# Kernel optimization log

Hardware: AMD Instinct MI355X
Metric: run time of the kernel (lower is better)

## Reference

```python
import jax, jax.numpy as jnp
import numpy as np

EPS = 1e-12

def _l2norm(x, axis=-1):
    n = jnp.sqrt(jnp.sum(x * x, axis=axis, keepdims=True))
    return x / jnp.maximum(n, EPS)

def setup_inputs() -> dict:
    key = jax.random.key(0)
    kq, kk, kv = jax.random.split(key, 3)
    N, K, D = 512, 262144, 256
    query = jax.random.normal(kq, (N, D), dtype=jnp.float32)
    # buffers are initialized as row-normalized gaussians in __init__
    queue_k = _l2norm(jax.random.normal(kk, (K, D), dtype=jnp.float32), axis=1)
    queue_v = _l2norm(jax.random.normal(kv, (K, D), dtype=jnp.float32), axis=1)
    return {"query": query, "queue_k": queue_k, "queue_v": queue_v}

TOP_N = 32

def reference(query, queue_k, queue_v):
    q = _l2norm(query.astype(jnp.float32), axis=1)          # [N, D]
    similarity = jnp.einsum('nd,kd->nk', q, queue_k)        # [N, K]
    _, topk_indices = jax.lax.top_k(similarity, TOP_N)      # [N, top_n]
    get_k = queue_k[topk_indices]                           # [N, top_n, D]
    get_v = queue_v[topk_indices]                           # [N, top_n, D]
    return (get_k, get_v)
```

## Files before the change

kernel.cpp:

```cpp
#include <hip/hip_runtime.h>
#include <hip/hip_bf16.h>

#define NQ     512
#define KTOT   262144
#define DD     256
#define TK     32
#define LSTR   264
#define NCHUNK 512
#define CHUNK  (KTOT / NCHUNK)
#define NTILE  (CHUNK / TK)
#define EMIT_T 0.189f
#define CAP    896
#define QCAP   8
#define NSLOT  (CAP / 64)
#define SEL    64
#define TOPN   32

typedef __bf16 bf16x8 __attribute__((ext_vector_type(8)));
typedef __bf16 bf16x4 __attribute__((ext_vector_type(4)));
typedef float  f32x4  __attribute__((ext_vector_type(4)));

__global__ void prep_kernel(const float* __restrict__ query,
                            __bf16* __restrict__ qn, int* __restrict__ cnt) {
    int q = blockIdx.x, l = threadIdx.x;
    f32x4 v = *(const f32x4*)&query[q * DD + l * 4];
    float ss = v.x*v.x + v.y*v.y + v.z*v.z + v.w*v.w;
    #pragma unroll
    for (int off = 32; off; off >>= 1) ss += __shfl_xor(ss, off);
    float s = rsqrtf(fmaxf(ss, 1e-24f));
    bf16x4 o = { (__bf16)(v.x * s), (__bf16)(v.y * s),
                 (__bf16)(v.z * s), (__bf16)(v.w * s) };
    *(bf16x4*)&qn[q * DD + l * 4] = o;
    if (l == 0) cnt[q] = 0;
}

__global__ __launch_bounds__(1024, 4)
void phase1_kernel(const __bf16* __restrict__ qn, const float* __restrict__ qk,
                   int* __restrict__ cnt, float* __restrict__ csc,
                   int* __restrict__ cix) {
    __shared__ __bf16 lds_k[2][TK * LSTR];
    __shared__ int    lcnt[NQ];
    __shared__ float  lsc[NQ][QCAP];
    __shared__ int    lkey[NQ][QCAP];
    const int tid  = threadIdx.x;
    const int lane = tid & 63, w = tid >> 6;
    const int am   = lane & 15, aq4 = lane >> 4;
    const size_t kbase = (size_t)blockIdx.x * CHUNK;
    const float* kp = &qk[kbase * DD];

    if (tid < NQ) lcnt[tid] = 0;

    bf16x8 areg[2][8];
    #pragma unroll
    for (int a = 0; a < 2; ++a)
        #pragma unroll
        for (int ds = 0; ds < 8; ++ds)
            areg[a][ds] = *(const bf16x8*)
                &qn[(w * 32 + a * 16 + am) * DD + ds * 32 + aq4 * 8];

    f32x4 r[2];

    auto loadt = [&](int t) {
        #pragma unroll
        for (int p = 0; p < 2; ++p)
            r[p] = *(const f32x4*)
                &kp[((size_t)t * TK + p * 16 + w) * DD + lane * 4];
    };

    auto staget = [&](int buf) {
        #pragma unroll
        for (int p = 0; p < 2; ++p) {
            bf16x4 o = { (__bf16)r[p].x, (__bf16)r[p].y,
                         (__bf16)r[p].z, (__bf16)r[p].w };
            *(bf16x4*)&lds_k[buf][(p * 16 + w) * LSTR + lane * 4] = o;
        }
    };

    auto bar = [&]() {
        __builtin_amdgcn_sched_barrier(0);
        asm volatile("s_waitcnt lgkmcnt(0)" ::: "memory");
        __builtin_amdgcn_s_barrier();
        __builtin_amdgcn_sched_barrier(0);
    };

    auto computet = [&](int t, int buf) {
        #pragma unroll
        for (int b = 0; b < 2; ++b) {
            bf16x8 bfr[8];
            #pragma unroll
            for (int ds = 0; ds < 8; ++ds)
                bfr[ds] = *(const bf16x8*)
                    &lds_k[buf][(b * 16 + am) * LSTR + ds * 32 + aq4 * 8];
            #pragma unroll
            for (int a = 0; a < 2; ++a) {
                f32x4 c = {0.f, 0.f, 0.f, 0.f};
                __builtin_amdgcn_s_setprio(1);
                #pragma unroll
                for (int ds = 0; ds < 8; ++ds)
                    c = __builtin_amdgcn_mfma_f32_16x16x32_bf16(
                            areg[a][ds], bfr[ds], c, 0, 0, 0);
                __builtin_amdgcn_s_setprio(0);
                bool hit = (c.x > EMIT_T) | (c.y > EMIT_T) |
                           (c.z > EMIT_T) | (c.w > EMIT_T);
                if (__ballot(hit)) {
                    #pragma unroll
                    for (int rr = 0; rr < 4; ++rr) {
                        float s = c[rr];
                        if (s > EMIT_T) {
                            int gq = w * 32 + a * 16 + aq4 * 4 + rr;
                            int gk = (int)kbase + t * TK + b * 16 + am;
                            int pos = atomicAdd(&lcnt[gq], 1);
                            if (pos < QCAP) {
                                lsc[gq][pos]  = s;
                                lkey[gq][pos] = gk;
                            } else {
                                int gp = atomicAdd(&cnt[gq], 1);
                                if (gp < CAP) {
                                    csc[gq * CAP + gp] = s;
                                    cix[gq * CAP + gp] = gk;
                                }
                            }
                        }
                    }
                }
            }
        }
    };

    loadt(0);
    staget(0);
    loadt(1);
    bar();

    #pragma unroll 1
    for (int t = 0; t < NTILE; ++t) {
        if (t + 1 < NTILE) {
            staget((t + 1) & 1);
            if (t + 2 < NTILE) loadt(t + 2);
        }
        computet(t, t & 1);
        bar();
    }

    if (tid < NQ) {
        int c = lcnt[tid]; c = c < QCAP ? c : QCAP;
        if (c) {
            int base = atomicAdd(&cnt[tid], c);
            for (int j = 0; j < c; ++j) {
                int pos = base + j;
                if (pos < CAP) {
                    csc[tid * CAP + pos] = lsc[tid][j];
                    cix[tid * CAP + pos] = lkey[tid][j];
                }
            }
        }
    }
}

__global__ __launch_bounds__(256)
void phase2_kernel(const float* __restrict__ query, const float* __restrict__ qk,
                   const float* __restrict__ qv, const int* __restrict__ cnt,
                   const float* __restrict__ csc, const int* __restrict__ cix,
                   float* __restrict__ out) {
    __shared__ float  s_sc[CAP];
    __shared__ int    s_ix[CAP];
    __shared__ float  qrow[DD];
    __shared__ double e_ex[SEL];
    __shared__ int    e_ix[SEL];
    __shared__ int    sel_ix[SEL];
    __shared__ int    topk[TOPN];
    const int q = blockIdx.x, tid = threadIdx.x;
    const int lane = tid & 63, w = tid >> 6;

    int n = cnt[q]; n = n < CAP ? n : CAP;
    for (int i = tid; i < n; i += 256) {
        s_sc[i] = csc[q * CAP + i];
        s_ix[i] = cix[q * CAP + i];
    }
    if (tid < 64) *(f32x4*)&qrow[tid * 4] = *(const f32x4*)&query[q * DD + tid * 4];
    if (tid < SEL) { e_ex[tid] = -1e300; e_ix[tid] = 0; sel_ix[tid] = 0; }
    __syncthreads();

    const int m = n < SEL ? n : SEL;

    if (w == 0) {
        float rs[NSLOT];
        #pragma unroll
        for (int slot = 0; slot < NSLOT; ++slot) {
            int i = slot * 64 + lane;
            rs[slot] = (i < n) ? s_sc[i] : -1e30f;
        }
        for (int j = 0; j < m; ++j) {
            float bv = -1e30f; int bslot = 0;
            #pragma unroll
            for (int slot = 0; slot < NSLOT; ++slot)
                if (rs[slot] > bv) { bv = rs[slot]; bslot = slot; }
            int bpay = (lane << 4) | bslot;
            #pragma unroll
            for (int off = 32; off; off >>= 1) {
                float ov = __shfl_down(bv, off);
                int   op = __shfl_down(bpay, off);
                if (ov > bv) { bv = ov; bpay = op; }
            }
            bpay = __shfl(bpay, 0);
            int wl = bpay >> 4, wslot = bpay & 15;
            if (lane == wl) rs[wslot] = -1e30f;
            if (lane == 0) sel_ix[j] = s_ix[wslot * 64 + wl];
        }
    }
    __syncthreads();

    for (int j = w; j < m; j += 4) {
        int idx = sel_ix[j];
        f32x4 kv  = *(const f32x4*)&qk[(size_t)idx * DD + lane * 4];
        f32x4 qv4 = *(const f32x4*)&qrow[lane * 4];
        double acc = (double)qv4.x * kv.x + (double)qv4.y * kv.y
                   + (double)qv4.z * kv.z + (double)qv4.w * kv.w;
        #pragma unroll
        for (int off = 32; off; off >>= 1) acc += __shfl_down(acc, off);
        if (lane == 0) { e_ex[j] = acc; e_ix[j] = idx; }
    }
    __syncthreads();

    if (w == 0) {
        double dv = e_ex[lane]; int di = e_ix[lane];
        for (int t = 0; t < TOPN; ++t) {
            double bv = dv; int bi = di; int bl = lane;
            #pragma unroll
            for (int off = 32; off; off >>= 1) {
                double ov = __shfl_down(bv, off);
                int    oi = __shfl_down(bi, off);
                int    ol = __shfl_down(bl, off);
                if (ov > bv || (ov == bv && oi < bi)) { bv = ov; bi = oi; bl = ol; }
            }
            bi = __shfl(bi, 0); bl = __shfl(bl, 0);
            if (lane == bl) dv = -1e300;
            if (lane == 0) topk[t] = bi;
        }
    }
    __syncthreads();

    #pragma unroll
    for (int f = tid; f < TOPN * 64; f += 256) {
        int j = f >> 6, c = (f & 63) * 4;
        int idx = topk[j];
        f32x4 kv = *(const f32x4*)&qk[(size_t)idx * DD + c];
        f32x4 vv = *(const f32x4*)&qv[(size_t)idx * DD + c];
        size_t o = (size_t)q * (TOPN * DD) + j * DD + c;
        *(f32x4*)&out[o] = kv;
        *(f32x4*)&out[(size_t)NQ * TOPN * DD + o] = vv;
    }
}

extern "C" void kernel_launch(void* const* d_in, const int* in_sizes, int n_in,
                              void* d_out, int out_size, void* d_ws, size_t ws_size,
                              hipStream_t stream) {
    const float* query = (const float*)d_in[0];
    const float* qk    = (const float*)d_in[1];
    const float* qv    = (const float*)d_in[2];
    float* out = (float*)d_out;

    char* ws = (char*)d_ws;
    int*    cnt = (int*)ws;
    __bf16* qn  = (__bf16*)(ws + 4096);
    float*  csc = (float*)(ws + 4096 + 262144);
    int*    cix = (int*)(ws + 4096 + 262144 + (size_t)NQ * CAP * 4);

    prep_kernel<<<NQ, 64, 0, stream>>>(query, qn, cnt);
    phase1_kernel<<<NCHUNK, 1024, 0, stream>>>(qn, qk, cnt, csc, cix);
    phase2_kernel<<<NQ, 256, 0, stream>>>(query, qk, qv, cnt, csc, cix, out);
}
```

Before: 557.6 us.

## Split phase1 blocks over query halves with 512-thread workgroups

Phase1 blocks now cover half of the queries (256) using 512 threads, and the grid grows to 2 x NCHUNK so each key chunk is processed by two blocks. Each block loads four rows per thread per tile instead of two, and a sched barrier is added after the global loads. Smaller workgroups with less LDS per block are meant to improve occupancy and scheduling flexibility. The cost is that every key chunk is read and converted to bf16 twice, doubling global reads of queue_k, though the second read may hit in cache.

```diff
diff --git a/kernel.cpp b/kernel.cpp
--- a/kernel.cpp
+++ b/kernel.cpp
@@ -9,6 +9,7 @@
 #define NCHUNK 512
 #define CHUNK  (KTOT / NCHUNK)
 #define NTILE  (CHUNK / TK)
+#define QBLK   256
 #define EMIT_T 0.189f
 #define CAP    896
 #define QCAP   8
@@ -34,21 +35,22 @@
     if (l == 0) cnt[q] = 0;
 }
 
-__global__ __launch_bounds__(1024, 4)
+__global__ __launch_bounds__(512, 4)
 void phase1_kernel(const __bf16* __restrict__ qn, const float* __restrict__ qk,
                    int* __restrict__ cnt, float* __restrict__ csc,
                    int* __restrict__ cix) {
     __shared__ __bf16 lds_k[2][TK * LSTR];
-    __shared__ int    lcnt[NQ];
-    __shared__ float  lsc[NQ][QCAP];
-    __shared__ int    lkey[NQ][QCAP];
+    __shared__ int    lcnt[QBLK];
+    __shared__ float  lsc[QBLK][QCAP];
+    __shared__ int    lkey[QBLK][QCAP];
     const int tid  = threadIdx.x;
     const int lane = tid & 63, w = tid >> 6;
     const int am   = lane & 15, aq4 = lane >> 4;
-    const size_t kbase = (size_t)blockIdx.x * CHUNK;
+    const int qh   = blockIdx.x;
+    const size_t kbase = (size_t)blockIdx.y * CHUNK;
     const float* kp = &qk[kbase * DD];
 
-    if (tid < NQ) lcnt[tid] = 0;
+    if (tid < QBLK) lcnt[tid] = 0;
 
     bf16x8 areg[2][8];
     #pragma unroll
@@ -56,23 +58,24 @@
         #pragma unroll
         for (int ds = 0; ds < 8; ++ds)
             areg[a][ds] = *(const bf16x8*)
-                &qn[(w * 32 + a * 16 + am) * DD + ds * 32 + aq4 * 8];
-
-    f32x4 r[2];
+                &qn[(qh * QBLK + w * 32 + a * 16 + am) * DD + ds * 32 + aq4 * 8];
+
+    f32x4 r[4];
 
     auto loadt = [&](int t) {
         #pragma unroll
-        for (int p = 0; p < 2; ++p)
+        for (int p = 0; p < 4; ++p)
             r[p] = *(const f32x4*)
-                &kp[((size_t)t * TK + p * 16 + w) * DD + lane * 4];
+                &kp[((size_t)t * TK + p * 8 + w) * DD + lane * 4];
+        __builtin_amdgcn_sched_barrier(0);
     };
 
     auto staget = [&](int buf) {
         #pragma unroll
-        for (int p = 0; p < 2; ++p) {
+        for (int p = 0; p < 4; ++p) {
             bf16x4 o = { (__bf16)r[p].x, (__bf16)r[p].y,
                          (__bf16)r[p].z, (__bf16)r[p].w };
-            *(bf16x4*)&lds_k[buf][(p * 16 + w) * LSTR + lane * 4] = o;
+            *(bf16x4*)&lds_k[buf][(p * 8 + w) * LSTR + lane * 4] = o;
         }
     };
 
@@ -107,13 +110,14 @@
                     for (int rr = 0; rr < 4; ++rr) {
                         float s = c[rr];
                         if (s > EMIT_T) {
-                            int gq = w * 32 + a * 16 + aq4 * 4 + rr;
+                            int lq = w * 32 + a * 16 + aq4 * 4 + rr;
                             int gk = (int)kbase + t * TK + b * 16 + am;
-                            int pos = atomicAdd(&lcnt[gq], 1);
+                            int pos = atomicAdd(&lcnt[lq], 1);
                             if (pos < QCAP) {
-                                lsc[gq][pos]  = s;
-                                lkey[gq][pos] = gk;
+                                lsc[lq][pos]  = s;
+                                lkey[lq][pos] = gk;
                             } else {
+                                int gq = qh * QBLK + lq;
                                 int gp = atomicAdd(&cnt[gq], 1);
                                 if (gp < CAP) {
                                     csc[gq * CAP + gp] = s;
@@ -142,15 +146,16 @@
         bar();
     }
 
-    if (tid < NQ) {
+    if (tid < QBLK) {
         int c = lcnt[tid]; c = c < QCAP ? c : QCAP;
         if (c) {
-            int base = atomicAdd(&cnt[tid], c);
+            int gq = qh * QBLK + tid;
+            int base = atomicAdd(&cnt[gq], c);
             for (int j = 0; j < c; ++j) {
                 int pos = base + j;
                 if (pos < CAP) {
-                    csc[tid * CAP + pos] = lsc[tid][j];
-                    cix[tid * CAP + pos] = lkey[tid][j];
+                    csc[gq * CAP + pos] = lsc[tid][j];
+                    cix[gq * CAP + pos] = lkey[tid][j];
                 }
             }
         }
@@ -267,6 +272,6 @@
     int*    cix = (int*)(ws + 4096 + 262144 + (size_t)NQ * CAP * 4);
 
     prep_kernel<<<NQ, 64, 0, stream>>>(query, qn, cnt);
-    phase1_kernel<<<NCHUNK, 1024, 0, stream>>>(qn, qk, cnt, csc, cix);
+    phase1_kernel<<<dim3(2, NCHUNK), 512, 0, stream>>>(qn, qk, cnt, csc, cix);
     phase2_kernel<<<NQ, 256, 0, stream>>>(query, qk, qv, cnt, csc, cix, out);
 }
```

New measurement: 589.0 us. 5.6% more time.
